# Optimization experiments

Hardware: AMD Instinct MI355X
Metric: run time of the kernel (lower is better)

Reference implementation:

```python
import jax, jax.numpy as jnp
import numpy as np

D = 4
KERNEL = (3, 3, 3, 3)
CIN = 8
COUT = 16
SPATIAL = (24, 24, 24, 24)
B = 8


def setup_inputs() -> dict:
    key = jax.random.key(0)
    k1, k2, k3 = jax.random.split(key, 3)
    x = jax.random.normal(k1, (B, CIN) + SPATIAL, dtype=jnp.float32)
    kmul = int(np.prod(KERNEL))  # 81
    # torch layout: zeros(O, kmul, 1).repeat(1,1,Cin).reshape(O, kmul*Cin)
    # -> flat dim is kernel-major, channel-minor
    weight = jax.random.normal(k2, (COUT, kmul * CIN), dtype=jnp.float32) * 0.05
    bias = jax.random.normal(k3, (COUT,), dtype=jnp.float32) * 0.05
    return {"x": x, "weight": weight, "bias": bias}


def reference(x, weight, bias):
    # Unflatten weight to (O, k1, k2, k3, k4, Cin) matching the unfold's
    # (kernel..., channel) flatten order, then run a direct 4-D 'same' conv
    # (cross-correlation, identical math to the unfold+matmul original).
    w = weight.reshape((COUT,) + KERNEL + (CIN,))
    dn = jax.lax.ConvDimensionNumbers(
        lhs_spec=(0, 1, 2, 3, 4, 5),   # N, C, s1..s4
        rhs_spec=(0, 5, 1, 2, 3, 4),   # O, I, k1..k4  (I lives at axis 5 of w)
        out_spec=(0, 1, 2, 3, 4, 5),   # N, O, s1..s4
    )
    out = jax.lax.conv_general_dilated(
        x, w,
        window_strides=(1,) * D,
        padding=[(1, 1)] * D,
        dimension_numbers=dn,
    )
    return out + bias.reshape((1, COUT) + (1,) * D)
```

## Files before the change

### kernel.cpp

```cpp
#include <hip/hip_runtime.h>
#include <hip/hip_bf16.h>


#define SDIM  24
#define SP    (SDIM * SDIM * SDIM * SDIM)
#define PD    26
#define SPPAD (PD * PD * PD * PD)
#define CIN   8
#define COUT  16
#define BATCH 8
#define KW    648
#define NCHUNK 21
#define NB    4
#define PTILES (SP / 16)
#define NBLOCKS ((BATCH / NB) * PTILES / 4)

#define ZERO_OFF 0
#define WPK_OFF  256
#define XT_OFF   32768
#define XT_BYTES  ((size_t)BATCH * SP * CIN * 2)
#define XTP_BYTES ((size_t)BATCH * SPPAD * CIN * 2)
#define WS_NEEDED_OLD (XT_OFF + XT_BYTES)
#define WS_NEEDED_PAD (XT_OFF + XTP_BYTES)

#define ZTOTAL ((size_t)BATCH * SPPAD)
#define ZBLOCKS 14281

typedef __attribute__((ext_vector_type(8))) short short8;
typedef __attribute__((ext_vector_type(4))) float f32x4;

static __device__ __forceinline__ unsigned short f2bf(float f) {
    unsigned u = __builtin_bit_cast(unsigned, f);
    u = (u + 0x7fffu + ((u >> 16) & 1u)) >> 16;
    return (unsigned short)u;
}

__global__ __launch_bounds__(256) void prep0_pad(
    const float* __restrict__ w, unsigned char* __restrict__ ws)
{
    if (blockIdx.x < ZBLOCKS) {
        size_t i = (size_t)blockIdx.x * 256 + threadIdx.x;
        if (i < ZTOTAL) {
            short8 z = {0, 0, 0, 0, 0, 0, 0, 0};
            ((short8*)(ws + XT_OFF))[i] = z;
        }
        return;
    }
    int t = (blockIdx.x - ZBLOCKS) * 256 + threadIdx.x;
    if (t >= NCHUNK * 64) return;
    int chunk = t >> 6;
    int lane  = t & 63;
    int m     = lane & 15;
    int quad  = lane >> 4;
    short8 pk;
    #pragma unroll
    for (int j = 0; j < 8; ++j) {
        int k = chunk * 32 + quad * 8 + j;
        float f = (k < KW) ? w[m * KW + k] : 0.0f;
        pk[j] = (short)f2bf(f);
    }
    ((short8*)(ws + WPK_OFF))[chunk * 64 + lane] = pk;
}

__global__ __launch_bounds__(256) void transpose_xp(
    const float* __restrict__ x, unsigned char* __restrict__ ws)
{
    int idx = blockIdx.x * 256 + threadIdx.x;
    int b  = idx / (SP / 4);
    int pq = idx - b * (SP / 4);
    int p  = pq * 4;
    const float* xb = x + (size_t)b * CIN * SP + p;

    float4 v[CIN];
    #pragma unroll
    for (int c = 0; c < CIN; ++c)
        v[c] = *(const float4*)(xb + (size_t)c * SP);

    union { __hip_bfloat162 h2[4]; short8 s8; } u[4];
    #pragma unroll
    for (int j = 0; j < 4; ++j) {
        #pragma unroll
        for (int i = 0; i < 4; ++i) {
            float a0 = (&v[2 * i].x)[j];
            float a1 = (&v[2 * i + 1].x)[j];
            u[j].h2[i] = __float22bfloat162_rn(make_float2(a0, a1));
        }
    }

    int r = p;
    const int p4 = r % SDIM; r /= SDIM;
    const int p3 = r % SDIM; r /= SDIM;
    const int p2 = r % SDIM;
    const int p1 = r / SDIM;
    int qp = (((p1 + 1) * PD + (p2 + 1)) * PD + (p3 + 1)) * PD + (p4 + 1);

    short8* dst = (short8*)(ws + XT_OFF) + (size_t)b * SPPAD + qp;
    #pragma unroll
    for (int j = 0; j < 4; ++j) dst[j] = u[j].s8;
}

__global__ __launch_bounds__(256) void conv4d_mfma_pad(
    const unsigned char* __restrict__ ws,
    const float* __restrict__ bias,
    float* __restrict__ out)
{
    __shared__ int    s_delta[96];
    __shared__ short8 s_w[NCHUNK * 64];

    const int tid  = threadIdx.x;
    const int lane = tid & 63;
    const int wave = tid >> 6;
    const int col  = lane & 15;
    const int quad = lane >> 4;

    const short8* wpk = (const short8*)(ws + WPK_OFF);
    for (int t = tid; t < NCHUNK * 64; t += 256) s_w[t] = wpk[t];
    if (tid < 84) {
        int k1 = tid / 27, rem = tid - k1 * 27;
        int k2 = rem / 9;  rem -= k2 * 9;
        int k3 = rem / 3;
        int k4 = rem - k3 * 3;
        s_delta[tid] = (k1 * (PD * PD * PD) + k2 * (PD * PD) + k3 * PD + k4) * 16;
    }
    __syncthreads();

    int W = blockIdx.x * 4 + wave;
    W = __builtin_amdgcn_readfirstlane(W);
    const int pt = W % PTILES;
    const int g  = W / PTILES;

    const int p = pt * 16 + col;
    int r = p;
    const int p4 = r % SDIM; r /= SDIM;
    const int p3 = r % SDIM; r /= SDIM;
    const int p2 = r % SDIM;
    const int p1 = r / SDIM;
    const int pidx16 = (((p1 * PD + p2) * PD + p3) * PD + p4) * 16;

    const unsigned char* xbase[NB];
    #pragma unroll
    for (int t = 0; t < NB; ++t)
        xbase[t] = ws + XT_OFF + (size_t)(g * NB + t) * SPPAD * 16;

    f32x4 acc[NB];
    #pragma unroll
    for (int t = 0; t < NB; ++t) acc[t] = (f32x4){0.f, 0.f, 0.f, 0.f};

    #pragma unroll
    for (int c = 0; c < NCHUNK; ++c) {
        short8 afrag = s_w[c * 64 + lane];
        int voff = pidx16 + s_delta[c * 4 + quad];

        short8 bf[NB];
        #pragma unroll
        for (int t = 0; t < NB; ++t)
            bf[t] = *(const short8*)(xbase[t] + voff);
        #pragma unroll
        for (int t = 0; t < NB; ++t)
            acc[t] = __builtin_amdgcn_mfma_f32_16x16x32_bf16(afrag, bf[t], acc[t], 0, 0, 0);
    }

    f32x4 b4 = *(const f32x4*)(bias + quad * 4);
    #pragma unroll
    for (int t = 0; t < NB; ++t) {
        float* obase = out + ((size_t)(g * NB + t) * COUT + quad * 4) * SP + p;
        #pragma unroll
        for (int reg = 0; reg < 4; ++reg)
            obase[(size_t)reg * SP] = acc[t][reg] + b4[reg];
    }
}


__global__ __launch_bounds__(256) void pack_weights(
    const float* __restrict__ w, unsigned char* __restrict__ ws)
{
    int t = blockIdx.x * 256 + threadIdx.x;
    if (t == 1344) {
        short8 z = {0,0,0,0,0,0,0,0};
        *(short8*)(ws + ZERO_OFF) = z;
    }
    if (t >= NCHUNK * 64) return;
    int chunk = t >> 6;
    int lane  = t & 63;
    int m     = lane & 15;
    int quad  = lane >> 4;
    short8 pk;
    #pragma unroll
    for (int j = 0; j < 8; ++j) {
        int k = chunk * 32 + quad * 8 + j;
        float f = (k < KW) ? w[m * KW + k] : 0.0f;
        pk[j] = (short)f2bf(f);
    }
    ((short8*)(ws + WPK_OFF))[chunk * 64 + lane] = pk;
}

__global__ __launch_bounds__(256) void transpose_x(
    const float* __restrict__ x, unsigned char* __restrict__ ws)
{
    int idx = blockIdx.x * 256 + threadIdx.x;
    int b  = idx / (SP / 2);
    int pp = idx - b * (SP / 2);
    int p  = pp * 2;
    const float* xb = x + (size_t)b * CIN * SP + p;

    float2 v[CIN];
    #pragma unroll
    for (int c = 0; c < CIN; ++c)
        v[c] = *(const float2*)(xb + (size_t)c * SP);

    union { __hip_bfloat162 h2[4]; short8 s8; } u0, u1;
    #pragma unroll
    for (int i = 0; i < 4; ++i) {
        float2 a = make_float2(v[2 * i].x, v[2 * i + 1].x);
        float2 bq = make_float2(v[2 * i].y, v[2 * i + 1].y);
        u0.h2[i] = __float22bfloat162_rn(a);
        u1.h2[i] = __float22bfloat162_rn(bq);
    }
    short8* dst = (short8*)(ws + XT_OFF) + ((size_t)b * SP + p);
    dst[0] = u0.s8;
    dst[1] = u1.s8;
}

__global__ __launch_bounds__(256) void conv4d_mfma(
    const unsigned char* __restrict__ ws,
    const float* __restrict__ bias,
    float* __restrict__ out)
{
    const int lane = threadIdx.x & 63;
    const int wave = threadIdx.x >> 6;
    const int col  = lane & 15;
    const int quad = lane >> 4;

    int W = blockIdx.x * 4 + wave;
    W = __builtin_amdgcn_readfirstlane(W);
    const int pt = W % PTILES;
    const int g  = W / PTILES;

    const int p = pt * 16 + col;
    int r = p;
    const int p4 = r % SDIM; r /= SDIM;
    const int p3 = r % SDIM; r /= SDIM;
    const int p2 = r % SDIM;
    const int p1 = r / SDIM;

    const short8* wpk  = (const short8*)(ws + WPK_OFF);
    const short8* xT   = (const short8*)(ws + XT_OFF);
    const short8* zslt = (const short8*)(ws + ZERO_OFF);

    const short8* xb[NB];
    #pragma unroll
    for (int t = 0; t < NB; ++t)
        xb[t] = xT + (size_t)(g * NB + t) * SP;

    f32x4 acc[NB];
    #pragma unroll
    for (int t = 0; t < NB; ++t) acc[t] = (f32x4){0.f, 0.f, 0.f, 0.f};

    #pragma unroll
    for (int c = 0; c < NCHUNK; ++c) {
        short8 afrag = wpk[c * 64 + lane];

        int tap = c * 4 + quad;
        int k1 = tap / 27; int rem = tap - k1 * 27;
        int k2 = rem / 9;  rem -= k2 * 9;
        int k3 = rem / 3;
        int k4 = rem - k3 * 3;
        int q1 = p1 + k1 - 1, q2 = p2 + k2 - 1, q3 = p3 + k3 - 1, q4 = p4 + k4 - 1;
        bool valid = ((unsigned)q1 < (unsigned)SDIM) & ((unsigned)q2 < (unsigned)SDIM) &
                     ((unsigned)q3 < (unsigned)SDIM) & ((unsigned)q4 < (unsigned)SDIM);
        int q = ((q1 * SDIM + q2) * SDIM + q3) * SDIM + q4;

        short8 bf[NB];
        #pragma unroll
        for (int t = 0; t < NB; ++t) {
            const short8* src = valid ? (xb[t] + q) : zslt;
            bf[t] = *src;
        }
        #pragma unroll
        for (int t = 0; t < NB; ++t)
            acc[t] = __builtin_amdgcn_mfma_f32_16x16x32_bf16(afrag, bf[t], acc[t], 0, 0, 0);
    }

    f32x4 b4 = *(const f32x4*)(bias + quad * 4);
    #pragma unroll
    for (int t = 0; t < NB; ++t) {
        float* obase = out + ((size_t)(g * NB + t) * COUT + quad * 4) * SP + p;
        #pragma unroll
        for (int reg = 0; reg < 4; ++reg)
            obase[(size_t)reg * SP] = acc[t][reg] + b4[reg];
    }
}

__global__ __launch_bounds__(256) void conv4d_direct(
    const float* __restrict__ x, const float* __restrict__ w,
    const float* __restrict__ bias, float* __restrict__ out)
{
    int t = blockIdx.x * blockDim.x + threadIdx.x;
    int b = t / SP;
    int p = t - b * SP;
    int p4 = p % SDIM; int tmp = p / SDIM;
    int p3 = tmp % SDIM; tmp /= SDIM;
    int p2 = tmp % SDIM; int p1 = tmp / SDIM;
    float acc[COUT];
    #pragma unroll
    for (int o = 0; o < COUT; ++o) acc[o] = bias[o];
    const float* xb = x + (size_t)b * CIN * SP;
    for (int k1 = 0; k1 < 3; ++k1) {
        unsigned q1 = (unsigned)(p1 + k1 - 1); if (q1 >= SDIM) continue;
        for (int k2 = 0; k2 < 3; ++k2) {
            unsigned q2 = (unsigned)(p2 + k2 - 1); if (q2 >= SDIM) continue;
            for (int k3 = 0; k3 < 3; ++k3) {
                unsigned q3 = (unsigned)(p3 + k3 - 1); if (q3 >= SDIM) continue;
                int base123 = (((int)q1 * SDIM + (int)q2) * SDIM + (int)q3) * SDIM;
                int kf = ((k1 * 3 + k2) * 3 + k3) * 3;
                for (int k4 = 0; k4 < 3; ++k4) {
                    unsigned q4 = (unsigned)(p4 + k4 - 1); if (q4 >= SDIM) continue;
                    int q = base123 + (int)q4;
                    float xv[CIN];
                    #pragma unroll
                    for (int c = 0; c < CIN; ++c) xv[c] = xb[c * SP + q];
                    const float* wp = w + (kf + k4) * CIN;
                    #pragma unroll
                    for (int o = 0; o < COUT; ++o)
                        #pragma unroll
                        for (int c = 0; c < CIN; ++c)
                            acc[o] = fmaf(xv[c], wp[o * KW + c], acc[o]);
                }
            }
        }
    }
    float* ob = out + (size_t)b * COUT * SP + p;
    #pragma unroll
    for (int o = 0; o < COUT; ++o) ob[o * SP] = acc[o];
}

extern "C" void kernel_launch(void* const* d_in, const int* in_sizes, int n_in,
                              void* d_out, int out_size, void* d_ws, size_t ws_size,
                              hipStream_t stream)
{
    const float* x    = (const float*)d_in[0];
    const float* w    = (const float*)d_in[1];
    const float* bias = (const float*)d_in[2];
    float* out        = (float*)d_out;
    unsigned char* ws = (unsigned char*)d_ws;

    if (ws_size >= WS_NEEDED_PAD) {
        hipLaunchKernelGGL(prep0_pad, dim3(ZBLOCKS + 6), dim3(256), 0, stream, w, ws);
        hipLaunchKernelGGL(transpose_xp, dim3(BATCH * SP / 4 / 256), dim3(256), 0, stream,
                           x, ws);
        hipLaunchKernelGGL(conv4d_mfma_pad, dim3(NBLOCKS), dim3(256), 0, stream,
                           (const unsigned char*)ws, bias, out);
        return;
    }

    if (ws_size >= WS_NEEDED_OLD) {
        hipLaunchKernelGGL(pack_weights, dim3(6), dim3(256), 0, stream, w, ws);
        const int pair_total = BATCH * SP / 2;
        hipLaunchKernelGGL(transpose_x, dim3(pair_total / 256), dim3(256), 0, stream, x, ws);
        hipLaunchKernelGGL(conv4d_mfma, dim3(NBLOCKS), dim3(256), 0, stream,
                           (const unsigned char*)ws, bias, out);
        return;
    }

    const int total = BATCH * SP;
    hipLaunchKernelGGL(conv4d_direct, dim3(total / 256), dim3(256), 0, stream,
                       x, w, bias, out);
}
```

Measured before the change: 350.3 us.

## Zero only halo slots, fuse prep kernels, and double-buffer conv input loads

```diff
diff --git a/kernel.cpp b/kernel.cpp
--- a/kernel.cpp
+++ b/kernel.cpp
@@ -23,8 +23,13 @@
 #define WS_NEEDED_OLD (XT_OFF + XT_BYTES)
 #define WS_NEEDED_PAD (XT_OFF + XTP_BYTES)
 
-#define ZTOTAL ((size_t)BATCH * SPPAD)
-#define ZBLOCKS 14281
+#define HALO_PER_B   125200
+#define HROW_SLOTS   97552
+#define HALO_TOTAL   (BATCH * HALO_PER_B)
+#define HBLOCKS      3913
+#define TBLOCKS      (BATCH * SP / 4 / 256)
+#define WBLOCKS      6
+#define PREP_BLOCKS  (HBLOCKS + TBLOCKS + WBLOCKS)
 
 typedef __attribute__((ext_vector_type(8))) short short8;
 typedef __attribute__((ext_vector_type(4))) float f32x4;
@@ -35,18 +40,91 @@
     return (unsigned short)u;
 }
 
-__global__ __launch_bounds__(256) void prep0_pad(
-    const float* __restrict__ w, unsigned char* __restrict__ ws)
-{
-    if (blockIdx.x < ZBLOCKS) {
-        size_t i = (size_t)blockIdx.x * 256 + threadIdx.x;
-        if (i < ZTOTAL) {
-            short8 z = {0, 0, 0, 0, 0, 0, 0, 0};
-            ((short8*)(ws + XT_OFF))[i] = z;
+__global__ __launch_bounds__(256) void prep_fused(
+    const float* __restrict__ x, const float* __restrict__ w,
+    unsigned char* __restrict__ ws)
+{
+    const int bid = blockIdx.x;
+    const int tid = threadIdx.x;
+
+    if (bid < HBLOCKS) {
+        int t = bid * 256 + tid;
+        if (t >= HALO_TOTAL) return;
+        int b = t / HALO_PER_B;
+        int h = t - b * HALO_PER_B;
+        int q1, q2, q3, q4;
+        if (h < HROW_SLOTS) {
+            int rid = h / 26;
+            q4 = h - rid * 26;
+            if (rid < 1352) {
+                q1 = (rid < 676) ? 0 : 25;
+                int rr = rid % 676;
+                q2 = rr / 26; q3 = rr - (rr / 26) * 26;
+            } else if (rid < 2600) {
+                int r2 = rid - 1352;
+                q1 = 1 + r2 / 52;
+                int rr = r2 - (r2 / 52) * 52;
+                q2 = (rr < 26) ? 0 : 25;
+                q3 = rr % 26;
+            } else {
+                int r3 = rid - 2600;
+                q1 = 1 + r3 / 48;
+                int rr = r3 - (r3 / 48) * 48;
+                q2 = 1 + rr / 2;
+                q3 = (rr & 1) ? 25 : 0;
+            }
+        } else {
+            int e = h - HROW_SLOTS;
+            int rid = e >> 1;
+            q4 = (e & 1) ? 25 : 0;
+            q1 = 1 + rid / 576;
+            int rr = rid - (rid / 576) * 576;
+            q2 = 1 + rr / 24;
+            q3 = 1 + rr - (rr / 24) * 24;
         }
+        size_t slot = (size_t)b * SPPAD + (((q1 * PD + q2) * PD + q3) * PD + q4);
+        short8 z = {0, 0, 0, 0, 0, 0, 0, 0};
+        ((short8*)(ws + XT_OFF))[slot] = z;
         return;
     }
-    int t = (blockIdx.x - ZBLOCKS) * 256 + threadIdx.x;
+
+    if (bid < HBLOCKS + TBLOCKS) {
+        int idx = (bid - HBLOCKS) * 256 + tid;
+        int b  = idx / (SP / 4);
+        int pq = idx - b * (SP / 4);
+        int p  = pq * 4;
+        const float* xb = x + (size_t)b * CIN * SP + p;
+
+        float4 v[CIN];
+        #pragma unroll
+        for (int c = 0; c < CIN; ++c)
+            v[c] = *(const float4*)(xb + (size_t)c * SP);
+
+        union { __hip_bfloat162 h2[4]; short8 s8; } u[4];
+        #pragma unroll
+        for (int j = 0; j < 4; ++j) {
+            #pragma unroll
+            for (int i = 0; i < 4; ++i) {
+                float a0 = (&v[2 * i].x)[j];
+                float a1 = (&v[2 * i + 1].x)[j];
+                u[j].h2[i] = __float22bfloat162_rn(make_float2(a0, a1));
+            }
+        }
+
+        int r = p;
+        const int p4 = r % SDIM; r /= SDIM;
+        const int p3 = r % SDIM; r /= SDIM;
+        const int p2 = r % SDIM;
+        const int p1 = r / SDIM;
+        int qp = (((p1 + 1) * PD + (p2 + 1)) * PD + (p3 + 1)) * PD + (p4 + 1);
+
+        short8* dst = (short8*)(ws + XT_OFF) + (size_t)b * SPPAD + qp;
+        #pragma unroll
+        for (int j = 0; j < 4; ++j) dst[j] = u[j].s8;
+        return;
+    }
+
+    int t = (bid - HBLOCKS - TBLOCKS) * 256 + tid;
     if (t >= NCHUNK * 64) return;
     int chunk = t >> 6;
     int lane  = t & 63;
@@ -60,43 +138,6 @@
         pk[j] = (short)f2bf(f);
     }
     ((short8*)(ws + WPK_OFF))[chunk * 64 + lane] = pk;
-}
-
-__global__ __launch_bounds__(256) void transpose_xp(
-    const float* __restrict__ x, unsigned char* __restrict__ ws)
-{
-    int idx = blockIdx.x * 256 + threadIdx.x;
-    int b  = idx / (SP / 4);
-    int pq = idx - b * (SP / 4);
-    int p  = pq * 4;
-    const float* xb = x + (size_t)b * CIN * SP + p;
-
-    float4 v[CIN];
-    #pragma unroll
-    for (int c = 0; c < CIN; ++c)
-        v[c] = *(const float4*)(xb + (size_t)c * SP);
-
-    union { __hip_bfloat162 h2[4]; short8 s8; } u[4];
-    #pragma unroll
-    for (int j = 0; j < 4; ++j) {
-        #pragma unroll
-        for (int i = 0; i < 4; ++i) {
-            float a0 = (&v[2 * i].x)[j];
-            float a1 = (&v[2 * i + 1].x)[j];
-            u[j].h2[i] = __float22bfloat162_rn(make_float2(a0, a1));
-        }
-    }
-
-    int r = p;
-    const int p4 = r % SDIM; r /= SDIM;
-    const int p3 = r % SDIM; r /= SDIM;
-    const int p2 = r % SDIM;
-    const int p1 = r / SDIM;
-    int qp = (((p1 + 1) * PD + (p2 + 1)) * PD + (p3 + 1)) * PD + (p4 + 1);
-
-    short8* dst = (short8*)(ws + XT_OFF) + (size_t)b * SPPAD + qp;
-    #pragma unroll
-    for (int j = 0; j < 4; ++j) dst[j] = u[j].s8;
 }
 
 __global__ __launch_bounds__(256) void conv4d_mfma_pad(
@@ -142,22 +183,33 @@
     for (int t = 0; t < NB; ++t)
         xbase[t] = ws + XT_OFF + (size_t)(g * NB + t) * SPPAD * 16;
 
+    int voffs[NCHUNK];
+    #pragma unroll
+    for (int c = 0; c < NCHUNK; ++c)
+        voffs[c] = pidx16 + s_delta[c * 4 + quad];
+
     f32x4 acc[NB];
     #pragma unroll
     for (int t = 0; t < NB; ++t) acc[t] = (f32x4){0.f, 0.f, 0.f, 0.f};
 
+    short8 bf[2][NB];
+    #pragma unroll
+    for (int t = 0; t < NB; ++t)
+        bf[0][t] = *(const short8*)(xbase[t] + voffs[0]);
+
     #pragma unroll
     for (int c = 0; c < NCHUNK; ++c) {
+        const int cur = c & 1;
+        const int nxt = cur ^ 1;
+        if (c + 1 < NCHUNK) {
+            #pragma unroll
+            for (int t = 0; t < NB; ++t)
+                bf[nxt][t] = *(const short8*)(xbase[t] + voffs[c + 1]);
+        }
         short8 afrag = s_w[c * 64 + lane];
-        int voff = pidx16 + s_delta[c * 4 + quad];
-
-        short8 bf[NB];
         #pragma unroll
         for (int t = 0; t < NB; ++t)
-            bf[t] = *(const short8*)(xbase[t] + voff);
-        #pragma unroll
-        for (int t = 0; t < NB; ++t)
-            acc[t] = __builtin_amdgcn_mfma_f32_16x16x32_bf16(afrag, bf[t], acc[t], 0, 0, 0);
+            acc[t] = __builtin_amdgcn_mfma_f32_16x16x32_bf16(afrag, bf[cur][t], acc[t], 0, 0, 0);
     }
 
     f32x4 b4 = *(const f32x4*)(bias + quad * 4);
@@ -345,9 +397,8 @@
     unsigned char* ws = (unsigned char*)d_ws;
 
     if (ws_size >= WS_NEEDED_PAD) {
-        hipLaunchKernelGGL(prep0_pad, dim3(ZBLOCKS + 6), dim3(256), 0, stream, w, ws);
-        hipLaunchKernelGGL(transpose_xp, dim3(BATCH * SP / 4 / 256), dim3(256), 0, stream,
-                           x, ws);
+        hipLaunchKernelGGL(prep_fused, dim3(PREP_BLOCKS), dim3(256), 0, stream,
+                           x, w, ws);
         hipLaunchKernelGGL(conv4d_mfma_pad, dim3(NBLOCKS), dim3(256), 0, stream,
                            (const unsigned char*)ws, bias, out);
         return;
```

Result: no change. 356.7 us (+1.8%).
